# Kernel tuning notes

Hardware: AMD Instinct MI355X
Metric: run time of the kernel (lower is better)

## Reference

```python
import jax, jax.numpy as jnp
import numpy as np

# OPT-1.3b-like attention dims
B, S, E, NH, HD = 1, 2048, 2048, 32, 64
Q_BITS, R_BITS, BASE_GS, R_GS = 1, 3, 16, 16


def quotrem_fake_quantize(x, q_bits=Q_BITS, r_bits=R_BITS, base_gs=BASE_GS, r_gs=R_GS):
    r_max = 2 ** (r_bits - 1) - 1
    r_min = -r_max - 1
    eps = 1e-8
    shape = x.shape
    H = shape[-1]
    xg = x.reshape(shape[:-1] + (H // base_gs, base_gs))  # [..., G_base, base_gs]
    max_abs = jnp.maximum(jnp.max(jnp.abs(xg), axis=-1, keepdims=True), eps)
    if q_bits == 1:
        log2_max = jnp.log2(max_abs)
        base_floor = jnp.exp2(jnp.floor(log2_max))
        base_ceil = jnp.exp2(jnp.ceil(log2_max))
        base = jnp.where(jnp.abs(max_abs - base_floor) <= jnp.abs(base_ceil - max_abs),
                         base_floor, base_ceil)
        base = jnp.clip(base, 1.0, 128.0)
        max_pos = jnp.max(xg, axis=-1, keepdims=True)
        min_val = jnp.min(xg, axis=-1, keepdims=True)
        sign_flag = jnp.where(jnp.abs(max_pos) >= jnp.abs(min_val), 1.0, -1.0)
        q = (xg * sign_flag >= base / 2.0).astype(x.dtype)
        q_scaled = q * sign_flag * base
    else:
        q_max = 2 ** (q_bits - 1) - 1
        threshold = max_abs / q_max
        base = jnp.full_like(threshold, 64.0)
        for b in (32.0, 16.0, 8.0, 4.0, 2.0):
            base = jnp.where(threshold <= b, jnp.full_like(threshold, b), base)
        q = jnp.clip(jnp.round(xg / base), -q_max, q_max)
        q_scaled = q * base
    r = (xg - q_scaled).reshape(shape)
    rg = r.reshape(shape[:-1] + (H // r_gs, r_gs))  # [..., G_r, r_gs]
    max_abs_r = jnp.maximum(jnp.max(jnp.abs(rg), axis=-1, keepdims=True), eps)
    scale_r = max_abs_r / r_max
    r_q = jnp.clip(jnp.round(rg / scale_r), r_min, r_max)
    r_dq = (r_q * scale_r).reshape(shape)
    return q_scaled.reshape(shape) + r_dq


def setup_inputs() -> dict:
    key = jax.random.key(0)
    ks = jax.random.split(key, 9)
    w = lambda k: jax.random.normal(k, (E, E), dtype=jnp.float32) * 0.02
    b = lambda k: jax.random.normal(k, (E,), dtype=jnp.float32) * 0.02
    return {
        "hidden_states": jax.random.normal(ks[0], (B, S, E), dtype=jnp.float32),
        "Wq": w(ks[1]), "bq": b(ks[2]),
        "Wk": w(ks[3]), "bk": b(ks[4]),
        "Wv": w(ks[5]), "bv": b(ks[6]),
        "Wo": w(ks[7]), "bo": b(ks[8]),
    }


def reference(hidden_states, Wq, bq, Wk, bk, Wv, bv, Wo, bo):
    scaling = HD ** -0.5
    heads = lambda x: x.reshape(B, S, NH, HD).transpose(0, 2, 1, 3)  # [B,NH,S,HD]
    q = heads((hidden_states @ Wq.T + bq) * scaling)
    k = quotrem_fake_quantize(heads(hidden_states @ Wk.T + bk))
    v = quotrem_fake_quantize(heads(hidden_states @ Wv.T + bv))
    scores = jnp.einsum('bhqd,bhkd->bhqk', q, k)
    idx = jnp.arange(S)
    scores = jnp.where(idx[:, None] >= idx[None, :], scores, -jnp.inf)  # causal
    attn = jax.nn.softmax(scores, axis=-1)
    out = jnp.einsum('bhqk,bhkd->bhqd', attn, v).transpose(0, 2, 1, 3).reshape(B, S, E)
    return out @ Wo.T + bo
```

## Files before the change

kernel.cpp:

```cpp
#include <hip/hip_runtime.h>
#include <math.h>

#define SEQ 2048
#define EMB 2048
#define NHEAD 32
#define HDIM 64

typedef unsigned short u16;
typedef _Float16 half8 __attribute__((ext_vector_type(8)));
typedef _Float16 half4 __attribute__((ext_vector_type(4)));
typedef __attribute__((ext_vector_type(4))) float floatx4;

__device__ __forceinline__ floatx4 mfma_f16(half8 a, half8 b, floatx4 c) {
    return __builtin_amdgcn_mfma_f32_16x16x32_f16(a, b, c, 0, 0, 0);
}
__device__ __forceinline__ void load16(const u16* g, u16* l) {
    __builtin_amdgcn_global_load_lds(
        (const __attribute__((address_space(1))) unsigned int*)g,
        (__attribute__((address_space(3))) unsigned int*)l, 16, 0, 0);
}
__device__ __forceinline__ u16 h2u(_Float16 h) { return *reinterpret_cast<u16*>(&h); }

__global__ __launch_bounds__(256)
void cvt4(const float* __restrict__ X0, u16* __restrict__ Y0,
          const float* __restrict__ X1, u16* __restrict__ Y1,
          const float* __restrict__ X2, u16* __restrict__ Y2,
          const float* __restrict__ X3, u16* __restrict__ Y3)
{
    const float* Xs[4] = {X0, X1, X2, X3};
    u16* Ys[4] = {Y0, Y1, Y2, Y3};
    const float* X = Xs[blockIdx.y];
    u16* Y = Ys[blockIdx.y];
    const int i = (blockIdx.x * 256 + threadIdx.x) * 4;
    float4 v = *reinterpret_cast<const float4*>(X + i);
    half4 hv;
    hv.x = (_Float16)v.x; hv.y = (_Float16)v.y;
    hv.z = (_Float16)v.z; hv.w = (_Float16)v.w;
    *reinterpret_cast<half4*>(Y + i) = hv;
}

__global__ __launch_bounds__(512, 2)
void gemm256(const u16* __restrict__ A,
             const u16* __restrict__ B0, const u16* __restrict__ B1,
             const u16* __restrict__ B2,
             const float* __restrict__ bk, const float* __restrict__ bv,
             const float* __restrict__ bq,
             float* __restrict__ F0, float* __restrict__ F1,
             u16* __restrict__ Qb)
{
    __shared__ __align__(16) u16 As[2][256 * 64];
    __shared__ __align__(16) u16 Bs[2][256 * 64];

    const int tid = threadIdx.x;
    const int w = tid >> 6, lane = tid & 63;
    const int wm = w >> 2, wn = w & 3;
    const int quad = lane >> 4, colk = lane & 15;
    const int lrow = lane >> 3, lphy = lane & 7;
    const int lsLog = (lphy - lrow) & 7;
    const int bn = blockIdx.x, bm = blockIdx.y, z = blockIdx.z;

    const u16* Bg  = (z == 0) ? B0 : (z == 1) ? B1 : B2;
    const u16* Ag  = A  + (size_t)(bm * 256 + lrow) * EMB + lsLog * 8;
    const u16* Bgp = Bg + (size_t)(bn * 256 + lrow) * EMB + lsLog * 8;

    const int kp0 = ((quad + colk) & 7) * 8;
    const int kp1 = ((quad + 4 + colk) & 7) * 8;
    int arow[8], brow[4];
    #pragma unroll
    for (int i = 0; i < 8; ++i) arow[i] = (wm * 128 + 16 * i + colk) * 64;
    #pragma unroll
    for (int j = 0; j < 4; ++j) brow[j] = (wn * 64 + 16 * j + colk) * 64;

    floatx4 acc[8][4];
    #pragma unroll
    for (int i = 0; i < 8; ++i)
        #pragma unroll
        for (int j = 0; j < 4; ++j) acc[i][j] = (floatx4){0.f, 0.f, 0.f, 0.f};

#define STAGE_A(MQ, BUF, KT) {                                                \
    _Pragma("unroll") for (int p_ = 0; p_ < 2; ++p_) {                        \
        const int r0_ = 128 * p_ + (MQ) * 64 + w * 8;                         \
        load16(Ag + (size_t)r0_ * EMB + (KT), &As[BUF][r0_ * 64 + lane * 8]); \
    } }
#define STAGE_B(NQ, BUF, KT) {                                                \
    _Pragma("unroll") for (int p_ = 0; p_ < 2; ++p_) {                        \
        const int b_ = w + 8 * p_;                                            \
        const int r0_ = 64 * (b_ >> 2) + (NQ) * 32 + (b_ & 3) * 8;            \
        load16(Bgp + (size_t)r0_ * EMB + (KT), &Bs[BUF][r0_ * 64 + lane * 8]);\
    } }

#define PHASE(MQ, NQ, BUF, STAGE, GUARD) {                                    \
    half8 af[4][2], bf[2][2];                                                 \
    _Pragma("unroll") for (int ii = 0; ii < 4; ++ii) {                        \
        const u16* ap_ = &As[BUF][arow[4 * (MQ) + ii]];                       \
        af[ii][0] = *reinterpret_cast<const half8*>(ap_ + kp0);               \
        af[ii][1] = *reinterpret_cast<const half8*>(ap_ + kp1);               \
    }                                                                         \
    _Pragma("unroll") for (int jj = 0; jj < 2; ++jj) {                        \
        const u16* bp_ = &Bs[BUF][brow[2 * (NQ) + jj]];                       \
        bf[jj][0] = *reinterpret_cast<const half8*>(bp_ + kp0);               \
        bf[jj][1] = *reinterpret_cast<const half8*>(bp_ + kp1);               \
    }                                                                         \
    STAGE                                                                     \
    __builtin_amdgcn_s_barrier();                                             \
    asm volatile("s_waitcnt lgkmcnt(0)" ::: "memory");                        \
    __builtin_amdgcn_s_setprio(1);                                            \
    _Pragma("unroll") for (int ii = 0; ii < 4; ++ii)                          \
        _Pragma("unroll") for (int jj = 0; jj < 2; ++jj) {                    \
            acc[4*(MQ)+ii][2*(NQ)+jj] =                                       \
                mfma_f16(af[ii][0], bf[jj][0], acc[4*(MQ)+ii][2*(NQ)+jj]);    \
            acc[4*(MQ)+ii][2*(NQ)+jj] =                                       \
                mfma_f16(af[ii][1], bf[jj][1], acc[4*(MQ)+ii][2*(NQ)+jj]);    \
        }                                                                     \
    __builtin_amdgcn_s_setprio(0);                                            \
    if (GUARD) asm volatile("s_waitcnt vmcnt(4)" ::: "memory");               \
    __builtin_amdgcn_s_barrier();                                             \
    __builtin_amdgcn_sched_barrier(0);                                        \
}

    STAGE_B(0, 0, 0)
    STAGE_A(0, 0, 0)
    STAGE_A(1, 0, 0)
    STAGE_B(1, 0, 0)
    STAGE_B(0, 1, 64)
    STAGE_A(0, 1, 64)
    asm volatile("s_waitcnt vmcnt(4)" ::: "memory");
    __builtin_amdgcn_s_barrier();
    __builtin_amdgcn_sched_barrier(0);

    #pragma unroll 1
    for (int it = 0; it < 16; ++it) {
        const int k1 = ((2 * it + 1) & 31) * 64;
        const int k2 = ((2 * it + 2) & 31) * 64;
        const int k3 = ((2 * it + 3) & 31) * 64;
        PHASE(0, 0, 0, STAGE_A(1, 1, k1), 0)
        PHASE(1, 0, 0, STAGE_B(1, 1, k1), 0)
        PHASE(0, 1, 0, STAGE_B(0, 0, k2), 0)
        PHASE(1, 1, 0, STAGE_A(0, 0, k2), 1)
        PHASE(0, 0, 1, STAGE_A(1, 0, k2), 0)
        PHASE(1, 0, 1, STAGE_B(1, 0, k2), 0)
        PHASE(0, 1, 1, STAGE_B(0, 1, k3), 0)
        PHASE(1, 1, 1, STAGE_A(0, 1, k3), 1)
    }
    asm volatile("s_waitcnt vmcnt(0)" ::: "memory");

#undef STAGE_A
#undef STAGE_B
#undef PHASE

    const float* bias = (z == 0) ? bk : (z == 1) ? bv : bq;
    #pragma unroll
    for (int i = 0; i < 8; ++i) {
        const int row = bm * 256 + wm * 128 + 16 * i + 4 * quad;
        #pragma unroll
        for (int j = 0; j < 4; ++j) {
            const int col = bn * 256 + wn * 64 + 16 * j + colk;
            const float bb = bias[col];
            #pragma unroll
            for (int r = 0; r < 4; ++r) {
                const size_t idx = (size_t)(row + r) * EMB + col;
                if (z == 2)
                    ((_Float16*)Qb)[idx] = (_Float16)((acc[i][j][r] + bb) * 0.125f);
                else
                    ((z == 0) ? F0 : F1)[idx] = acc[i][j][r] + bb;
            }
        }
    }
}

__global__ __launch_bounds__(256)
void gemm16(const u16* __restrict__ A,
            const u16* __restrict__ B0, const u16* __restrict__ B1,
            const u16* __restrict__ B2,
            const float* __restrict__ bk, const float* __restrict__ bv,
            const float* __restrict__ bq,
            float* __restrict__ F0, float* __restrict__ F1,
            u16* __restrict__ Qb)
{
    __shared__ __align__(16) u16 As[128 * 64];
    __shared__ __align__(16) u16 Bs[128 * 64];

    const int tid = threadIdx.x;
    const int w = tid >> 6, lane = tid & 63;
    const int quad = lane >> 4, colk = lane & 15;
    const int bn = blockIdx.x, bm = blockIdx.y, z = blockIdx.z;
    const int wm = (w & 1) * 64, wn = (w >> 1) * 64;

    const u16* Bg = (z == 0) ? B0 : (z == 1) ? B1 : B2;

    const int srow = tid >> 3, sphy = tid & 7;
    const int sLog = (sphy - srow) & 7;
    size_t agof[4], bgof[4];
    int ldst[4];
    #pragma unroll
    for (int p = 0; p < 4; ++p) {
        const int row = srow + 32 * p;
        agof[p] = (size_t)(bm * 128 + row) * EMB + sLog * 8;
        bgof[p] = (size_t)(bn * 128 + row) * EMB + sLog * 8;
        ldst[p] = (tid + 256 * p) * 8;
    }

    const int aoct0 = ((quad + colk) & 7) * 8;
    const int aoct1 = ((quad + 4 + colk) & 7) * 8;

    floatx4 acc[4][4];
    #pragma unroll
    for (int i = 0; i < 4; ++i)
        #pragma unroll
        for (int j = 0; j < 4; ++j) acc[i][j] = (floatx4){0.f, 0.f, 0.f, 0.f};

    for (int kt = 0; kt < 2048; kt += 64) {
        __syncthreads();
        #pragma unroll
        for (int p = 0; p < 4; ++p) {
            load16(A  + agof[p] + kt, As + ldst[p]);
            load16(Bg + bgof[p] + kt, Bs + ldst[p]);
        }
        __syncthreads();

        half8 a0[4], a1[4], b0[4], b1[4];
        #pragma unroll
        for (int i = 0; i < 4; ++i) {
            a0[i] = *reinterpret_cast<const half8*>(&As[(wm + 16*i + colk) * 64 + aoct0]);
            a1[i] = *reinterpret_cast<const half8*>(&As[(wm + 16*i + colk) * 64 + aoct1]);
        }
        #pragma unroll
        for (int j = 0; j < 4; ++j) {
            b0[j] = *reinterpret_cast<const half8*>(&Bs[(wn + 16*j + colk) * 64 + aoct0]);
            b1[j] = *reinterpret_cast<const half8*>(&Bs[(wn + 16*j + colk) * 64 + aoct1]);
        }
        #pragma unroll
        for (int i = 0; i < 4; ++i)
            #pragma unroll
            for (int j = 0; j < 4; ++j) {
                acc[i][j] = mfma_f16(a0[i], b0[j], acc[i][j]);
                acc[i][j] = mfma_f16(a1[i], b1[j], acc[i][j]);
            }
    }

    const float* bias = (z == 0) ? bk : (z == 1) ? bv : bq;
    #pragma unroll
    for (int i = 0; i < 4; ++i) {
        const int row = bm * 128 + wm + 16*i + 4*quad;
        #pragma unroll
        for (int j = 0; j < 4; ++j) {
            const int col = bn * 128 + wn + 16*j + colk;
            const float bv2 = bias[col];
            #pragma unroll
            for (int r = 0; r < 4; ++r) {
                const size_t idx = (size_t)(row + r) * EMB + col;
                if (z == 2)
                    ((_Float16*)Qb)[idx] = (_Float16)((acc[i][j][r] + bv2) * 0.125f);
                else
                    ((z == 0) ? F0 : F1)[idx] = acc[i][j][r] + bv2;
            }
        }
    }
}

__device__ __forceinline__ void quotrem16(float* x)
{
    float maxabs = 1e-8f, maxpos = -INFINITY, minval = INFINITY;
    #pragma unroll
    for (int i = 0; i < 16; ++i) {
        maxabs = fmaxf(maxabs, fabsf(x[i]));
        maxpos = fmaxf(maxpos, x[i]);
        minval = fminf(minval, x[i]);
    }
    const float lg = log2f(maxabs);
    const float bfl = exp2f(floorf(lg));
    const float bcl = exp2f(ceilf(lg));
    float base = (fabsf(maxabs - bfl) <= fabsf(bcl - maxabs)) ? bfl : bcl;
    base = fminf(fmaxf(base, 1.0f), 128.0f);
    const float sgn = (fabsf(maxpos) >= fabsf(minval)) ? 1.0f : -1.0f;
    const float hb = 0.5f * base, sb = sgn * base;

    float qs[16], r[16], maxr = 1e-8f;
    #pragma unroll
    for (int i = 0; i < 16; ++i) {
        qs[i] = (x[i] * sgn >= hb) ? sb : 0.0f;
        r[i]  = x[i] - qs[i];
        maxr  = fmaxf(maxr, fabsf(r[i]));
    }
    const float scale = maxr / 3.0f;
    #pragma unroll
    for (int i = 0; i < 16; ++i) {
        float rq = rintf(r[i] / scale);
        rq = fminf(fmaxf(rq, -4.0f), 3.0f);
        x[i] = qs[i] + rq * scale;
    }
}

__global__ __launch_bounds__(256)
void quant_kv(const float* __restrict__ FK, u16* __restrict__ Kb,
              const float* __restrict__ FV, u16* __restrict__ Vt,
              const float* __restrict__ Wo, u16* __restrict__ Wo16)
{
    __shared__ u16 T[64 * 264];
    const int bid = blockIdx.x, t = threadIdx.x;

    if (bid >= 1280) {
        const int i = ((bid - 1280) * 256 + t) * 4;
        float4 v = *reinterpret_cast<const float4*>(Wo + i);
        half4 hv;
        hv.x = (_Float16)v.x; hv.y = (_Float16)v.y;
        hv.z = (_Float16)v.z; hv.w = (_Float16)v.w;
        *reinterpret_cast<half4*>(Wo16 + i) = hv;
        return;
    }

    if (bid < 1024) {
        const int g = bid * 256 + t;
        const float* p = FK + (size_t)g * 16;
        float x[16];
        #pragma unroll
        for (int i = 0; i < 16; i += 4)
            *reinterpret_cast<float4*>(&x[i]) = *reinterpret_cast<const float4*>(p + i);
        quotrem16(x);
        _Float16* o = (_Float16*)Kb + (size_t)g * 16;
        #pragma unroll
        for (int i = 0; i < 16; ++i) o[i] = (_Float16)x[i];
        return;
    }

    const int l = bid - 1024;
    const int sb = l >> 5, h = l & 31;
    const float* src = FV + (size_t)(sb * 256 + t) * EMB + h * HDIM;

    #pragma unroll
    for (int g4 = 0; g4 < 4; ++g4) {
        float x[16];
        #pragma unroll
        for (int i = 0; i < 16; i += 4)
            *reinterpret_cast<float4*>(&x[i]) =
                *reinterpret_cast<const float4*>(src + g4 * 16 + i);
        quotrem16(x);
        #pragma unroll
        for (int i = 0; i < 16; ++i)
            T[(g4 * 16 + i) * 264 + t] = h2u((_Float16)x[i]);
    }
    __syncthreads();

    const int d = t >> 2, seg = t & 3;
    u16* dst = Vt + (size_t)(h * HDIM + d) * SEQ + sb * 256 + seg * 64;
    #pragma unroll
    for (int jj = 0; jj < 8; ++jj)
        *reinterpret_cast<half8*>(dst + jj * 8) =
            *reinterpret_cast<const half8*>(&T[d * 264 + seg * 64 + jj * 8]);
}

__global__ __launch_bounds__(512)
void flash128(const u16* __restrict__ Qb, const u16* __restrict__ Kb,
              const u16* __restrict__ Vt, u16* __restrict__ Ob)
{
    __shared__ __align__(16) u16 Ks[2][128 * 64];
    __shared__ __align__(16) u16 Vs[2][64 * 128];
    __shared__ __align__(16) u16 Ps[128 * 136];

    const int tid = threadIdx.x;
    const int w = tid >> 6, lane = tid & 63;
    const int wg = w >> 2, wl = w & 3;
    const int quad = lane >> 4, colk = lane & 15;
    const int id = blockIdx.x;
    const int h = (id & 7) * 4 + ((id >> 3) & 3);
    const int pairb = id >> 5;

    int krow[2], koff[2], vd[2], voff[2], ldst[2];
    #pragma unroll
    for (int p = 0; p < 2; ++p) {
        const int c = tid + p * 512;
        krow[p] = c >> 3;
        koff[p] = (((c & 7) - krow[p]) & 7) * 8;
        vd[p]   = c >> 4;
        voff[p] = (((c & 15) - vd[p]) & 15) * 8;
        ldst[p] = c * 8;
    }
    const int kp0 = ((quad + colk) & 7) * 8;
    const int kp1 = ((quad + 4 + colk) & 7) * 8;
    const int rloc = wg * 64 + 16 * wl + colk;

#define STAGEKV(KW, BUF) {                                                     \
    _Pragma("unroll") for (int p_ = 0; p_ < 2; ++p_) {                         \
        load16(Kb + (size_t)((KW) * 128 + krow[p_]) * EMB + h * HDIM + koff[p_],\
               &Ks[BUF][ldst[p_]]);                                            \
        load16(Vt + (size_t)(h * HDIM + vd[p_]) * SEQ + (KW) * 128 + voff[p_], \
               &Vs[BUF][ldst[p_]]);                                            \
    } }

    #pragma unroll
    for (int pass = 0; pass < 2; ++pass) {
        const int qt = pass ? (15 - pairb) : pairb;
        const int nw = qt + 1;
        const int qrow_g = qt * 128 + rloc;

        const half8 qb0 = *reinterpret_cast<const half8*>(
            &Qb[(size_t)qrow_g * EMB + h * HDIM + quad * 8]);
        const half8 qb1 = *reinterpret_cast<const half8*>(
            &Qb[(size_t)qrow_g * EMB + h * HDIM + 32 + quad * 8]);

        STAGEKV(0, 0)

        floatx4 o[4];
        #pragma unroll
        for (int t = 0; t < 4; ++t) o[t] = (floatx4){0.f, 0.f, 0.f, 0.f};
        float lsum = 0.f;
        int cur = 0;

        #pragma unroll 1
        for (int kw = 0; kw < nw; ++kw) {
            if (kw + 1 < nw) {
                STAGEKV(kw + 1, cur ^ 1)
                asm volatile("s_waitcnt vmcnt(4)" ::: "memory");
            } else {
                asm volatile("s_waitcnt vmcnt(0)" ::: "memory");
            }
            __builtin_amdgcn_s_barrier();
            __builtin_amdgcn_sched_barrier(0);

            floatx4 s[8];
            #pragma unroll
            for (int t = 0; t < 8; ++t) {
                const half8 kb0 = *reinterpret_cast<const half8*>(&Ks[cur][(16*t + colk) * 64 + kp0]);
                const half8 kb1 = *reinterpret_cast<const half8*>(&Ks[cur][(16*t + colk) * 64 + kp1]);
                floatx4 zz = (floatx4){0.f, 0.f, 0.f, 0.f};
                zz = mfma_f16(kb0, qb0, zz);
                s[t] = mfma_f16(kb1, qb1, zz);
            }
            if (kw == nw - 1) {
                #pragma unroll
                for (int t = 0; t < 8; ++t)
                    #pragma unroll
                    for (int r = 0; r < 4; ++r)
                        if (kw * 128 + 16*t + 4*quad + r > qrow_g) s[t][r] = -INFINITY;
            }

            #pragma unroll
            for (int t = 0; t < 8; ++t) {
                half4 pw;
                float pv0 = __expf(s[t][0] - 4.0f), pv1 = __expf(s[t][1] - 4.0f);
                float pv2 = __expf(s[t][2] - 4.0f), pv3 = __expf(s[t][3] - 4.0f);
                lsum += (pv0 + pv1) + (pv2 + pv3);
                pw.x = (_Float16)pv0; pw.y = (_Float16)pv1;
                pw.z = (_Float16)pv2; pw.w = (_Float16)pv3;
                *reinterpret_cast<half4*>(&Ps[rloc * 136 + 16*t + 4*quad]) = pw;
            }

            half8 pa[4];
            #pragma unroll
            for (int seg = 0; seg < 4; ++seg)
                pa[seg] = *reinterpret_cast<const half8*>(&Ps[rloc * 136 + seg * 32 + quad * 8]);
            #pragma unroll
            for (int t = 0; t < 4; ++t) {
                #pragma unroll
                for (int seg = 0; seg < 4; ++seg) {
                    const int vp = ((4*seg + quad + colk) & 15) * 8;
                    const half8 vb = *reinterpret_cast<const half8*>(&Vs[cur][(16*t + colk) * 128 + vp]);
                    o[t] = mfma_f16(pa[seg], vb, o[t]);
                }
            }

            __builtin_amdgcn_s_barrier();
            __builtin_amdgcn_sched_barrier(0);
            cur ^= 1;
        }

        lsum += __shfl_xor(lsum, 16, 64);
        lsum += __shfl_xor(lsum, 32, 64);

        float invr[4];
        #pragma unroll
        for (int r = 0; r < 4; ++r) invr[r] = 1.0f / __shfl(lsum, 4*quad + r, 64);
        #pragma unroll
        for (int t = 0; t < 4; ++t)
            #pragma unroll
            for (int r = 0; r < 4; ++r) {
                const int row = qt * 128 + wg * 64 + 16*wl + 4*quad + r;
                ((_Float16*)Ob)[(size_t)row * EMB + h * HDIM + 16*t + colk] =
                    (_Float16)(o[t][r] * invr[r]);
            }
    }
#undef STAGEKV
}

extern "C" void kernel_launch(void* const* d_in, const int* in_sizes, int n_in,
                              void* d_out, int out_size, void* d_ws, size_t ws_size,
                              hipStream_t stream)
{
    const float* hidden = (const float*)d_in[0];
    const float* Wq = (const float*)d_in[1];
    const float* bq = (const float*)d_in[2];
    const float* Wk = (const float*)d_in[3];
    const float* bk = (const float*)d_in[4];
    const float* Wv = (const float*)d_in[5];
    const float* bv = (const float*)d_in[6];
    const float* Wo = (const float*)d_in[7];
    const float* bo = (const float*)d_in[8];
    float* out = (float*)d_out;

    char* ws = (char*)d_ws;
    const size_t MB = 1024 * 1024;
    u16*   H16  = (u16*)(ws);
    u16*   Wk16 = (u16*)(ws + 8 * MB);
    u16*   Wv16 = (u16*)(ws + 16 * MB);
    float* FK   = (float*)(ws + 24 * MB);
    float* FV   = (float*)(ws + 40 * MB);
    u16*   Qbuf = (u16*)(ws + 56 * MB);
    u16*   Kbuf = (u16*)(ws + 8 * MB);
    u16*   Vtb  = (u16*)(ws + 16 * MB);
    u16*   Wo16 = (u16*)(ws);
    u16*   Obuf = (u16*)(ws + 24 * MB);
    u16*   Wq16 = (u16*)d_out;

    const dim3 cb(256);
    float* nilf = nullptr; u16* nil16 = nullptr;

    hipLaunchKernelGGL(cvt4, dim3(4096, 4), cb, 0, stream,
                       hidden, H16, Wk, Wk16, Wv, Wv16, Wq, Wq16);
    hipLaunchKernelGGL(gemm256, dim3(8, 8, 3), dim3(512), 0, stream,
                       H16, Wk16, Wv16, Wq16, bk, bv, bq, FK, FV, Qbuf);
    hipLaunchKernelGGL(quant_kv, dim3(1280 + 4096), cb, 0, stream,
                       FK, Kbuf, FV, Vtb, Wo, Wo16);
    hipLaunchKernelGGL(flash128, dim3(256), dim3(512), 0, stream,
                       Qbuf, Kbuf, Vtb, Obuf);
    hipLaunchKernelGGL(gemm16, dim3(16, 16, 1), cb, 0, stream,
                       Obuf, Wo16, nil16, nil16, bo, nilf, nilf,
                       out, nilf, nil16);
}
```

Baseline: 295.7 us.

## Fuse K/V quotrem quantization into projection GEMM epilogue and fold Wo conversion

Removes the separate quant_kv kernel. The K and V projection GEMM blocks now stage their fp32 accumulator tiles through swizzled LDS slabs, apply the quotient/remainder fake quantization in the epilogue, and write fp16 K and transposed V directly. This avoids writing and re-reading fp32 K/V intermediates. The Wo fp32-to-fp16 conversion moves into an extra z-slice of the GEMM grid. The trade-offs are a serialized 8-step epilogue with barriers and scattered 2-byte transposed V stores, which may be uncoalesced.

```diff
diff --git a/kernel.cpp b/kernel.cpp
--- a/kernel.cpp
+++ b/kernel.cpp
@@ -20,6 +20,39 @@
         (__attribute__((address_space(3))) unsigned int*)l, 16, 0, 0);
 }
 __device__ __forceinline__ u16 h2u(_Float16 h) { return *reinterpret_cast<u16*>(&h); }
+
+__device__ __forceinline__ void quotrem16(float* x)
+{
+    float maxabs = 1e-8f, maxpos = -INFINITY, minval = INFINITY;
+    #pragma unroll
+    for (int i = 0; i < 16; ++i) {
+        maxabs = fmaxf(maxabs, fabsf(x[i]));
+        maxpos = fmaxf(maxpos, x[i]);
+        minval = fminf(minval, x[i]);
+    }
+    const float lg = log2f(maxabs);
+    const float bfl = exp2f(floorf(lg));
+    const float bcl = exp2f(ceilf(lg));
+    float base = (fabsf(maxabs - bfl) <= fabsf(bcl - maxabs)) ? bfl : bcl;
+    base = fminf(fmaxf(base, 1.0f), 128.0f);
+    const float sgn = (fabsf(maxpos) >= fabsf(minval)) ? 1.0f : -1.0f;
+    const float hb = 0.5f * base, sb = sgn * base;
+
+    float qs[16], r[16], maxr = 1e-8f;
+    #pragma unroll
+    for (int i = 0; i < 16; ++i) {
+        qs[i] = (x[i] * sgn >= hb) ? sb : 0.0f;
+        r[i]  = x[i] - qs[i];
+        maxr  = fmaxf(maxr, fabsf(r[i]));
+    }
+    const float scale = maxr / 3.0f;
+    #pragma unroll
+    for (int i = 0; i < 16; ++i) {
+        float rq = rintf(r[i] / scale);
+        rq = fminf(fmaxf(rq, -4.0f), 3.0f);
+        x[i] = qs[i] + rq * scale;
+    }
+}
 
 __global__ __launch_bounds__(256)
 void cvt4(const float* __restrict__ X0, u16* __restrict__ Y0,
@@ -45,19 +78,35 @@
              const u16* __restrict__ B2,
              const float* __restrict__ bk, const float* __restrict__ bv,
              const float* __restrict__ bq,
-             float* __restrict__ F0, float* __restrict__ F1,
+             const float* __restrict__ Wo, u16* __restrict__ Wo16,
+             u16* __restrict__ Kb, u16* __restrict__ Vt,
              u16* __restrict__ Qb)
 {
     __shared__ __align__(16) u16 As[2][256 * 64];
     __shared__ __align__(16) u16 Bs[2][256 * 64];
 
     const int tid = threadIdx.x;
+    const int bn = blockIdx.x, bm = blockIdx.y, z = blockIdx.z;
+
+    if (z == 3) {
+        const int b = bm * 8 + bn;
+        #pragma unroll
+        for (int c = 0; c < 32; ++c) {
+            const int i = ((c * 64 + b) * 512 + tid) * 4;
+            float4 v = *reinterpret_cast<const float4*>(Wo + i);
+            half4 hv;
+            hv.x = (_Float16)v.x; hv.y = (_Float16)v.y;
+            hv.z = (_Float16)v.z; hv.w = (_Float16)v.w;
+            *reinterpret_cast<half4*>(Wo16 + i) = hv;
+        }
+        return;
+    }
+
     const int w = tid >> 6, lane = tid & 63;
     const int wm = w >> 2, wn = w & 3;
     const int quad = lane >> 4, colk = lane & 15;
     const int lrow = lane >> 3, lphy = lane & 7;
     const int lsLog = (lphy - lrow) & 7;
-    const int bn = blockIdx.x, bm = blockIdx.y, z = blockIdx.z;
 
     const u16* Bg  = (z == 0) ? B0 : (z == 1) ? B1 : B2;
     const u16* Ag  = A  + (size_t)(bm * 256 + lrow) * EMB + lsLog * 8;
@@ -148,21 +197,72 @@
 #undef STAGE_B
 #undef PHASE
 
-    const float* bias = (z == 0) ? bk : (z == 1) ? bv : bq;
-    #pragma unroll
-    for (int i = 0; i < 8; ++i) {
-        const int row = bm * 256 + wm * 128 + 16 * i + 4 * quad;
-        #pragma unroll
-        for (int j = 0; j < 4; ++j) {
-            const int col = bn * 256 + wn * 64 + 16 * j + colk;
-            const float bb = bias[col];
-            #pragma unroll
-            for (int r = 0; r < 4; ++r) {
-                const size_t idx = (size_t)(row + r) * EMB + col;
-                if (z == 2)
+    if (z == 2) {
+        #pragma unroll
+        for (int i = 0; i < 8; ++i) {
+            const int row = bm * 256 + wm * 128 + 16 * i + 4 * quad;
+            #pragma unroll
+            for (int j = 0; j < 4; ++j) {
+                const int col = bn * 256 + wn * 64 + 16 * j + colk;
+                const float bb = bq[col];
+                #pragma unroll
+                for (int r = 0; r < 4; ++r) {
+                    const size_t idx = (size_t)(row + r) * EMB + col;
                     ((_Float16*)Qb)[idx] = (_Float16)((acc[i][j][r] + bb) * 0.125f);
-                else
-                    ((z == 0) ? F0 : F1)[idx] = acc[i][j][r] + bb;
+                }
+            }
+        }
+        return;
+    }
+
+    {
+        const float* bias = (z == 0) ? bk : bv;
+        float* slab = (float*)As;
+        #pragma unroll 1
+        for (int s = 0; s < 8; ++s) {
+            __syncthreads();
+            if (wm == (s >> 2)) {
+                #pragma unroll
+                for (int di = 0; di < 2; ++di) {
+                    const int i = 2 * (s & 3) + di;
+                    #pragma unroll
+                    for (int j = 0; j < 4; ++j) {
+                        const int cl = wn * 64 + 16 * j + colk;
+                        const float bb = bias[bn * 256 + cl];
+                        #pragma unroll
+                        for (int r = 0; r < 4; ++r) {
+                            const int rl = 16 * di + 4 * quad + r;
+                            slab[rl * 256 + (cl ^ ((rl & 7) << 2))] =
+                                acc[i][j][r] + bb;
+                        }
+                    }
+                }
+            }
+            __syncthreads();
+            {
+                const int rl = tid >> 4, grp = tid & 15;
+                const int swz = (rl & 7) << 2;
+                float x[16];
+                #pragma unroll
+                for (int c = 0; c < 4; ++c) {
+                    const int base = rl * 256 + ((grp * 16 + 4 * c) ^ swz);
+                    float4 v = *reinterpret_cast<const float4*>(&slab[base]);
+                    x[4*c+0] = v.x; x[4*c+1] = v.y;
+                    x[4*c+2] = v.z; x[4*c+3] = v.w;
+                }
+                quotrem16(x);
+                const int rowg = bm * 256 + s * 32 + rl;
+                const int colg = bn * 256 + grp * 16;
+                if (z == 0) {
+                    _Float16* o = (_Float16*)Kb + (size_t)rowg * EMB + colg;
+                    #pragma unroll
+                    for (int k = 0; k < 16; ++k) o[k] = (_Float16)x[k];
+                } else {
+                    #pragma unroll
+                    for (int k = 0; k < 16; ++k)
+                        ((_Float16*)Vt)[(size_t)(colg + k) * SEQ + rowg] =
+                            (_Float16)x[k];
+                }
             }
         }
     }
@@ -256,97 +356,6 @@
             }
         }
     }
-}
-
-__device__ __forceinline__ void quotrem16(float* x)
-{
-    float maxabs = 1e-8f, maxpos = -INFINITY, minval = INFINITY;
-    #pragma unroll
-    for (int i = 0; i < 16; ++i) {
-        maxabs = fmaxf(maxabs, fabsf(x[i]));
-        maxpos = fmaxf(maxpos, x[i]);
-        minval = fminf(minval, x[i]);
-    }
-    const float lg = log2f(maxabs);
-    const float bfl = exp2f(floorf(lg));
-    const float bcl = exp2f(ceilf(lg));
-    float base = (fabsf(maxabs - bfl) <= fabsf(bcl - maxabs)) ? bfl : bcl;
-    base = fminf(fmaxf(base, 1.0f), 128.0f);
-    const float sgn = (fabsf(maxpos) >= fabsf(minval)) ? 1.0f : -1.0f;
-    const float hb = 0.5f * base, sb = sgn * base;
-
-    float qs[16], r[16], maxr = 1e-8f;
-    #pragma unroll
-    for (int i = 0; i < 16; ++i) {
-        qs[i] = (x[i] * sgn >= hb) ? sb : 0.0f;
-        r[i]  = x[i] - qs[i];
-        maxr  = fmaxf(maxr, fabsf(r[i]));
-    }
-    const float scale = maxr / 3.0f;
-    #pragma unroll
-    for (int i = 0; i < 16; ++i) {
-        float rq = rintf(r[i] / scale);
-        rq = fminf(fmaxf(rq, -4.0f), 3.0f);
-        x[i] = qs[i] + rq * scale;
-    }
-}
-
-__global__ __launch_bounds__(256)
-void quant_kv(const float* __restrict__ FK, u16* __restrict__ Kb,
-              const float* __restrict__ FV, u16* __restrict__ Vt,
-              const float* __restrict__ Wo, u16* __restrict__ Wo16)
-{
-    __shared__ u16 T[64 * 264];
-    const int bid = blockIdx.x, t = threadIdx.x;
-
-    if (bid >= 1280) {
-        const int i = ((bid - 1280) * 256 + t) * 4;
-        float4 v = *reinterpret_cast<const float4*>(Wo + i);
-        half4 hv;
-        hv.x = (_Float16)v.x; hv.y = (_Float16)v.y;
-        hv.z = (_Float16)v.z; hv.w = (_Float16)v.w;
-        *reinterpret_cast<half4*>(Wo16 + i) = hv;
-        return;
-    }
-
-    if (bid < 1024) {
-        const int g = bid * 256 + t;
-        const float* p = FK + (size_t)g * 16;
-        float x[16];
-        #pragma unroll
-        for (int i = 0; i < 16; i += 4)
-            *reinterpret_cast<float4*>(&x[i]) = *reinterpret_cast<const float4*>(p + i);
-        quotrem16(x);
-        _Float16* o = (_Float16*)Kb + (size_t)g * 16;
-        #pragma unroll
-        for (int i = 0; i < 16; ++i) o[i] = (_Float16)x[i];
-        return;
-    }
-
-    const int l = bid - 1024;
-    const int sb = l >> 5, h = l & 31;
-    const float* src = FV + (size_t)(sb * 256 + t) * EMB + h * HDIM;
-
-    #pragma unroll
-    for (int g4 = 0; g4 < 4; ++g4) {
-        float x[16];
-        #pragma unroll
-        for (int i = 0; i < 16; i += 4)
-            *reinterpret_cast<float4*>(&x[i]) =
-                *reinterpret_cast<const float4*>(src + g4 * 16 + i);
-        quotrem16(x);
-        #pragma unroll
-        for (int i = 0; i < 16; ++i)
-            T[(g4 * 16 + i) * 264 + t] = h2u((_Float16)x[i]);
-    }
-    __syncthreads();
-
-    const int d = t >> 2, seg = t & 3;
-    u16* dst = Vt + (size_t)(h * HDIM + d) * SEQ + sb * 256 + seg * 64;
-    #pragma unroll
-    for (int jj = 0; jj < 8; ++jj)
-        *reinterpret_cast<half8*>(dst + jj * 8) =
-            *reinterpret_cast<const half8*>(&T[d * 264 + seg * 64 + jj * 8]);
 }
 
 __global__ __launch_bounds__(512)
@@ -502,27 +511,23 @@
     u16*   H16  = (u16*)(ws);
     u16*   Wk16 = (u16*)(ws + 8 * MB);
     u16*   Wv16 = (u16*)(ws + 16 * MB);
-    float* FK   = (float*)(ws + 24 * MB);
-    float* FV   = (float*)(ws + 40 * MB);
+    u16*   Kbuf = (u16*)(ws + 24 * MB);
+    u16*   Wo16 = (u16*)(ws + 32 * MB);
+    u16*   Vtb  = (u16*)(ws + 40 * MB);
     u16*   Qbuf = (u16*)(ws + 56 * MB);
-    u16*   Kbuf = (u16*)(ws + 8 * MB);
-    u16*   Vtb  = (u16*)(ws + 16 * MB);
-    u16*   Wo16 = (u16*)(ws);
-    u16*   Obuf = (u16*)(ws + 24 * MB);
+    u16*   Obuf = (u16*)(ws);
     u16*   Wq16 = (u16*)d_out;
 
-    const dim3 cb(256);
     float* nilf = nullptr; u16* nil16 = nullptr;
 
-    hipLaunchKernelGGL(cvt4, dim3(4096, 4), cb, 0, stream,
+    hipLaunchKernelGGL(cvt4, dim3(4096, 4), dim3(256), 0, stream,
                        hidden, H16, Wk, Wk16, Wv, Wv16, Wq, Wq16);
-    hipLaunchKernelGGL(gemm256, dim3(8, 8, 3), dim3(512), 0, stream,
-                       H16, Wk16, Wv16, Wq16, bk, bv, bq, FK, FV, Qbuf);
-    hipLaunchKernelGGL(quant_kv, dim3(1280 + 4096), cb, 0, stream,
-                       FK, Kbuf, FV, Vtb, Wo, Wo16);
+    hipLaunchKernelGGL(gemm256, dim3(8, 8, 4), dim3(512), 0, stream,
+                       H16, Wk16, Wv16, Wq16, bk, bv, bq,
+                       Wo, Wo16, Kbuf, Vtb, Qbuf);
     hipLaunchKernelGGL(flash128, dim3(256), dim3(512), 0, stream,
                        Qbuf, Kbuf, Vtb, Obuf);
-    hipLaunchKernelGGL(gemm16, dim3(16, 16, 1), cb, 0, stream,
+    hipLaunchKernelGGL(gemm16, dim3(16, 16, 1), dim3(256), 0, stream,
                        Obuf, Wo16, nil16, nil16, bo, nilf, nilf,
                        out, nilf, nil16);
 }
```

New measurement: 328.7 us. 11.1% more time.
